# Kernel optimization log

Hardware: AMD Instinct MI355X
Metric: run time of the kernel (lower is better)

The kernel has to match this reference:

```python
import jax, jax.numpy as jnp
import numpy as np


def setup_inputs() -> dict:
    key = jax.random.key(0)
    ks = jax.random.split(key, 5)
    B, S, D, H, E = 2, 2048, 1024, 2816, 8
    x = jax.random.normal(ks[0], (B, S, D), dtype=jnp.float32)
    Wg = jax.random.normal(ks[1], (E, D), dtype=jnp.float32) * 0.02
    W1 = jax.random.normal(ks[2], (E, H, D), dtype=jnp.float32) * 0.02
    W2 = jax.random.normal(ks[3], (E, H, D), dtype=jnp.float32) * 0.02
    W3 = jax.random.normal(ks[4], (E, D, H), dtype=jnp.float32) * 0.02
    return {"x": x, "Wg": Wg, "W1": W1, "W2": W2, "W3": W3}


TOP_K = 2


def reference(x, Wg, W1, W2, W3):
    B, S, D = x.shape
    E = Wg.shape[0]
    xt = x.reshape(B * S, D)  # [T, D]
    # gating: raw logits, NO softmax (matches original module)
    scores = xt @ Wg.T  # [T, E]
    topk_scores, topk_idx = jax.lax.top_k(scores, TOP_K)  # [T, K]
    # dense per-expert SwiGLU FFN over all tokens, combined with sparse weights
    gate = jax.nn.silu(jnp.einsum('td,ehd->teh', xt, W1))  # [T, E, H]
    up = jnp.einsum('td,ehd->teh', xt, W2)                 # [T, E, H]
    y = jnp.einsum('teh,edh->ted', gate * up, W3)           # [T, E, D]
    # combine weights: w[t, e] = sum_k topk_scores[t, k] * (topk_idx[t, k] == e)
    onehot = jax.nn.one_hot(topk_idx, E, dtype=x.dtype)     # [T, K, E]
    w = jnp.einsum('tke,tk->te', onehot, topk_scores)       # [T, E]
    out = jnp.einsum('te,ted->td', w, y)                    # [T, D]
    return out.reshape(B, S, D)
```

## Files before the change

kernel.cpp:

```cpp
#include <hip/hip_runtime.h>
#include <hip/hip_bf16.h>
#include <stdint.h>


#define T_TOK 4096
#define DDIM 1024
#define HDIM 2816
#define NEXP 8

typedef __attribute__((ext_vector_type(8))) short short8;
typedef __attribute__((ext_vector_type(4))) short short4v;
typedef __attribute__((ext_vector_type(4))) float floatx4;

__device__ __forceinline__ short f2bf(float f) {
  union { float f; unsigned int u; } v; v.f = f;
  unsigned int u = v.u;
  u += 0x7FFFu + ((u >> 16) & 1u);
  return (short)(u >> 16);
}

__device__ __forceinline__ void gl2lds16(const void* g, void* l) {
  __builtin_amdgcn_global_load_lds(
      (const __attribute__((address_space(1))) void*)g,
      (__attribute__((address_space(3))) void*)l, 16, 0, 0);
}

#define CONV_ELEM4 5767168
__global__ __launch_bounds__(256) void convert_kernel(
    const float* __restrict__ W1, const float* __restrict__ W2, const float* __restrict__ W3,
    short* __restrict__ W1bf, short* __restrict__ W2bf, short* __restrict__ W3bf) {
  int z = blockIdx.y;
  const float4* src = (const float4*)((z == 0) ? W1 : (z == 1) ? W2 : W3);
  short4v* dst = (short4v*)((z == 0) ? W1bf : (z == 1) ? W2bf : W3bf);
  size_t stride = (size_t)gridDim.x * 256;
  for (size_t i = (size_t)blockIdx.x * 256 + threadIdx.x; i < CONV_ELEM4; i += stride) {
    float4 v = src[i];
    dst[i] = (short4v){f2bf(v.x), f2bf(v.y), f2bf(v.z), f2bf(v.w)};
  }
}

__global__ __launch_bounds__(256) void gating_score_kernel(const float* __restrict__ x,
    const float* __restrict__ Wg, short* __restrict__ xbf,
    int* __restrict__ re, float* __restrict__ rw) {
  int t = blockIdx.x * 4 + (threadIdx.x >> 6);
  int lane = threadIdx.x & 63;
  const float* xt = x + (size_t)t * DDIM;
  float xr[16];
#pragma unroll
  for (int j = 0; j < 16; ++j) xr[j] = xt[j * 64 + lane];
  short* xbt = xbf + (size_t)t * DDIM;
#pragma unroll
  for (int j = 0; j < 16; ++j) xbt[j * 64 + lane] = f2bf(xr[j]);
  float s[NEXP];
#pragma unroll
  for (int e = 0; e < NEXP; ++e) {
    const float* wge = Wg + e * DDIM;
    float p = 0.f;
#pragma unroll
    for (int j = 0; j < 16; ++j) p += xr[j] * wge[j * 64 + lane];
#pragma unroll
    for (int o = 32; o > 0; o >>= 1) p += __shfl_xor(p, o, 64);
    s[e] = p;
  }
  if (lane == 0) {
    int e1 = 0; float s1 = s[0];
#pragma unroll
    for (int e = 1; e < NEXP; ++e) if (s[e] > s1) { s1 = s[e]; e1 = e; }
    int e2 = -1; float s2 = -1e30f;
#pragma unroll
    for (int e = 0; e < NEXP; ++e) if (e != e1 && s[e] > s2) { s2 = s[e]; e2 = e; }
    re[2 * t] = e1;     rw[2 * t] = s1;
    re[2 * t + 1] = e2; rw[2 * t + 1] = s2;
  }
}

__global__ __launch_bounds__(1024) void route_kernel(const int* __restrict__ re,
    int* __restrict__ counts, int* __restrict__ offs,
    int* __restrict__ rs, int* __restrict__ tlist) {
  __shared__ int H[NEXP * 1024];
  __shared__ int totS[NEXP];
  int tid = threadIdx.x;
  int myre[8];
  int cnt[NEXP];
#pragma unroll
  for (int e = 0; e < NEXP; ++e) cnt[e] = 0;
  const int4* re4 = (const int4*)(re + tid * 8);
  int4 a = re4[0], b = re4[1];
  myre[0] = a.x; myre[1] = a.y; myre[2] = a.z; myre[3] = a.w;
  myre[4] = b.x; myre[5] = b.y; myre[6] = b.z; myre[7] = b.w;
#pragma unroll
  for (int j = 0; j < 8; ++j) cnt[myre[j]]++;
#pragma unroll
  for (int e = 0; e < NEXP; ++e) H[e * 1024 + tid] = cnt[e];
  __syncthreads();
  int wave = tid >> 6, lane = tid & 63;
  if (wave < NEXP) {
    int run = 0;
    for (int c = 0; c < 16; ++c) {
      int i = c * 64 + lane;
      int v = H[wave * 1024 + i];
      int sc = v;
#pragma unroll
      for (int o = 1; o < 64; o <<= 1) {
        int u = __shfl_up(sc, o, 64);
        if (lane >= o) sc += u;
      }
      int tot = __shfl(sc, 63, 64);
      H[wave * 1024 + i] = run + sc - v;
      run += tot;
    }
    if (lane == 0) totS[wave] = run;
  }
  __syncthreads();
  if (tid == 0) {
    int run = 0;
    for (int e = 0; e < NEXP; ++e) {
      offs[e] = run; counts[e] = totS[e]; run += totS[e];
    }
  }
  int pos[NEXP];
#pragma unroll
  for (int e = 0; e < NEXP; ++e) pos[e] = H[e * 1024 + tid];
#pragma unroll
  for (int j = 0; j < 8; ++j) {
    int e = myre[j];
    int slot = pos[e]++;
    int idx = tid * 8 + j;
    rs[idx] = slot;
    tlist[e * T_TOK + slot] = idx >> 1;
  }
}

__global__ __launch_bounds__(256) void ffn1_fast_kernel(const short* __restrict__ xbf,
    const short* __restrict__ W1bf, const short* __restrict__ W2bf,
    const int* __restrict__ counts, const int* __restrict__ offs,
    const int* __restrict__ tlist, short* __restrict__ hmat) {
  int e = blockIdx.z;
  int cnt = counts[e];
  int m0 = blockIdx.y * 128;
  if (m0 >= cnt) return;
  int n0 = blockIdx.x * 64;
  __shared__ __attribute__((aligned(16))) short As[128 * 64];
  __shared__ __attribute__((aligned(16))) short Bs1[64 * 64];
  __shared__ __attribute__((aligned(16))) short Bs2[64 * 64];
  __shared__ int toks[128];
  int tid = threadIdx.x;
  if (tid < 128) {
    int m = m0 + tid;
    toks[tid] = tlist[e * T_TOK + (m < cnt ? m : cnt - 1)];
  }
  __syncthreads();
  int lane = tid & 63, w = tid >> 6;
  int wr = w >> 1, wc = w & 1;
  int lrow = lane & 15, lq = lane >> 4;
  int sr = lane >> 3;
  int sc = lane & 7;
  int scs = ((sc ^ sr) & 7) * 8;
  const short* pA[4];
#pragma unroll
  for (int j = 0; j < 4; ++j)
    pA[j] = xbf + (size_t)toks[w * 32 + j * 8 + sr] * DDIM + scs;
  const short* b1e = W1bf + (size_t)e * HDIM * DDIM;
  const short* b2e = W2bf + (size_t)e * HDIM * DDIM;
  const short* pB1[2]; const short* pB2[2];
#pragma unroll
  for (int j = 0; j < 2; ++j) {
    int row = w * 16 + j * 8 + sr;
    pB1[j] = b1e + (size_t)(n0 + row) * DDIM + scs;
    pB2[j] = b2e + (size_t)(n0 + row) * DDIM + scs;
  }
  void* lA[4]; void* lB1[2]; void* lB2[2];
#pragma unroll
  for (int j = 0; j < 4; ++j) lA[j] = (void*)&As[(w * 32 + j * 8) * 64];
#pragma unroll
  for (int j = 0; j < 2; ++j) {
    lB1[j] = (void*)&Bs1[(w * 16 + j * 8) * 64];
    lB2[j] = (void*)&Bs2[(w * 16 + j * 8) * 64];
  }
  floatx4 accg[4][2], accu[4][2];
#pragma unroll
  for (int i = 0; i < 4; ++i)
#pragma unroll
    for (int j = 0; j < 2; ++j) {
      accg[i][j] = (floatx4){0.f, 0.f, 0.f, 0.f};
      accu[i][j] = (floatx4){0.f, 0.f, 0.f, 0.f};
    }
  for (int kk = 0; kk < DDIM; kk += 64) {
#pragma unroll
    for (int j = 0; j < 4; ++j) { gl2lds16(pA[j], lA[j]); pA[j] += 64; }
#pragma unroll
    for (int j = 0; j < 2; ++j) {
      gl2lds16(pB1[j], lB1[j]); pB1[j] += 64;
      gl2lds16(pB2[j], lB2[j]); pB2[j] += 64;
    }
    __syncthreads();
#pragma unroll
    for (int kh = 0; kh < 2; ++kh) {
      int csw = (((kh * 4 + lq) ^ (lrow & 7)) & 7) * 8;
      short8 a[4], b1[2], b2[2];
#pragma unroll
      for (int mf = 0; mf < 4; ++mf)
        a[mf] = *(short8*)&As[(wr * 64 + mf * 16 + lrow) * 64 + csw];
#pragma unroll
      for (int nf = 0; nf < 2; ++nf) {
        b1[nf] = *(short8*)&Bs1[(wc * 32 + nf * 16 + lrow) * 64 + csw];
        b2[nf] = *(short8*)&Bs2[(wc * 32 + nf * 16 + lrow) * 64 + csw];
      }
#pragma unroll
      for (int mf = 0; mf < 4; ++mf)
#pragma unroll
        for (int nf = 0; nf < 2; ++nf) {
          accg[mf][nf] = __builtin_amdgcn_mfma_f32_16x16x32_bf16(a[mf], b1[nf], accg[mf][nf], 0, 0, 0);
          accu[mf][nf] = __builtin_amdgcn_mfma_f32_16x16x32_bf16(a[mf], b2[nf], accu[mf][nf], 0, 0, 0);
        }
    }
    __syncthreads();
  }
  int base = offs[e];
#pragma unroll
  for (int mf = 0; mf < 4; ++mf)
#pragma unroll
    for (int r = 0; r < 4; ++r) {
      int mloc = wr * 64 + mf * 16 + lq * 4 + r;
      if (m0 + mloc < cnt) {
        size_t row = (size_t)(base + m0 + mloc);
#pragma unroll
        for (int nf = 0; nf < 2; ++nf) {
          float g = accg[mf][nf][r];
          float u = accu[mf][nf][r];
          float h = g / (1.f + __expf(-g)) * u;
          hmat[row * HDIM + n0 + wc * 32 + nf * 16 + lrow] = f2bf(h);
        }
      }
    }
}

#define KSPLIT 2
#define KHALF (HDIM / KSPLIT)
__global__ __launch_bounds__(256) void ffn2_fast_kernel(const short* __restrict__ hmat,
    const short* __restrict__ W3bf,
    const int* __restrict__ counts, const int* __restrict__ offs,
    float* __restrict__ ypart0, float* __restrict__ ypart1) {
  int e = blockIdx.z;
  int cnt = counts[e];
  int m0 = blockIdx.y * 128;
  if (m0 >= cnt) return;
  int ks = blockIdx.x >> 3;
  int n0 = (blockIdx.x & 7) * 128;
  int k0 = ks * KHALF;
  float* ypart = ks ? ypart1 : ypart0;
  int base = offs[e];
  __shared__ __attribute__((aligned(16))) short As[128 * 64];
  __shared__ __attribute__((aligned(16))) short Bs[128 * 64];
  int tid = threadIdx.x;
  int lane = tid & 63, w = tid >> 6;
  int wr = w >> 1, wc = w & 1;
  int lrow = lane & 15, lq = lane >> 4;
  int sr = lane >> 3;
  int sc = lane & 7;
  int scs = ((sc ^ sr) & 7) * 8;
  const short* W3e = W3bf + (size_t)e * DDIM * HDIM;
  const short* pA[4]; const short* pB[4];
  void* lA[4]; void* lB[4];
#pragma unroll
  for (int j = 0; j < 4; ++j) {
    int gr = m0 + w * 32 + j * 8 + sr;
    gr = gr < cnt ? gr : cnt - 1;
    pA[j] = hmat + (size_t)(base + gr) * HDIM + k0 + scs;
    pB[j] = W3e + (size_t)(n0 + w * 32 + j * 8 + sr) * HDIM + k0 + scs;
    lA[j] = (void*)&As[(w * 32 + j * 8) * 64];
    lB[j] = (void*)&Bs[(w * 32 + j * 8) * 64];
  }
  floatx4 acc[4][4];
#pragma unroll
  for (int i = 0; i < 4; ++i)
#pragma unroll
    for (int j = 0; j < 4; ++j) acc[i][j] = (floatx4){0.f, 0.f, 0.f, 0.f};
  for (int kk = 0; kk < KHALF; kk += 64) {
#pragma unroll
    for (int j = 0; j < 4; ++j) { gl2lds16(pA[j], lA[j]); pA[j] += 64; }
#pragma unroll
    for (int j = 0; j < 4; ++j) { gl2lds16(pB[j], lB[j]); pB[j] += 64; }
    __syncthreads();
#pragma unroll
    for (int kh = 0; kh < 2; ++kh) {
      int csw = (((kh * 4 + lq) ^ (lrow & 7)) & 7) * 8;
      short8 a[4], b[4];
#pragma unroll
      for (int mf = 0; mf < 4; ++mf)
        a[mf] = *(short8*)&As[(wr * 64 + mf * 16 + lrow) * 64 + csw];
#pragma unroll
      for (int nf = 0; nf < 4; ++nf)
        b[nf] = *(short8*)&Bs[(wc * 64 + nf * 16 + lrow) * 64 + csw];
#pragma unroll
      for (int mf = 0; mf < 4; ++mf)
#pragma unroll
        for (int nf = 0; nf < 4; ++nf)
          acc[mf][nf] = __builtin_amdgcn_mfma_f32_16x16x32_bf16(a[mf], b[nf], acc[mf][nf], 0, 0, 0);
    }
    __syncthreads();
  }
#pragma unroll
  for (int mf = 0; mf < 4; ++mf)
#pragma unroll
    for (int r = 0; r < 4; ++r) {
      int mloc = wr * 64 + mf * 16 + lq * 4 + r;
      if (m0 + mloc < cnt) {
        float* orow = ypart + (size_t)(base + m0 + mloc) * DDIM + n0 + wc * 64 + lrow;
#pragma unroll
        for (int nf = 0; nf < 4; ++nf)
          orow[nf * 16] = acc[mf][nf][r];
      }
    }
}

__global__ __launch_bounds__(256) void combine_kernel(const float4* __restrict__ y0,
    const float4* __restrict__ y1,
    const int* __restrict__ offs, const int* __restrict__ re, const int* __restrict__ rs,
    const float* __restrict__ rw, float4* __restrict__ out4) {
  int t = blockIdx.x;
  int i = threadIdx.x;
  size_t r0 = (size_t)(offs[re[2 * t]] + rs[2 * t]) * 256 + i;
  size_t r1 = (size_t)(offs[re[2 * t + 1]] + rs[2 * t + 1]) * 256 + i;
  float w0 = rw[2 * t], w1 = rw[2 * t + 1];
  float4 a0 = y0[r0], a1 = y1[r0];
  float4 b0 = y0[r1], b1 = y1[r1];
  out4[(size_t)t * 256 + i] = make_float4(
      w0 * (a0.x + a1.x) + w1 * (b0.x + b1.x),
      w0 * (a0.y + a1.y) + w1 * (b0.y + b1.y),
      w0 * (a0.z + a1.z) + w1 * (b0.z + b1.z),
      w0 * (a0.w + a1.w) + w1 * (b0.w + b1.w));
}

extern "C" void kernel_launch(void* const* d_in, const int* in_sizes, int n_in,
                              void* d_out, int out_size, void* d_ws, size_t ws_size,
                              hipStream_t stream) {
  const float* x  = (const float*)d_in[0];
  const float* Wg = (const float*)d_in[1];
  const float* W1 = (const float*)d_in[2];
  const float* W2 = (const float*)d_in[3];
  const float* W3 = (const float*)d_in[4];
  float* out = (float*)d_out;
  char* ws = (char*)d_ws;

  int*   counts = (int*)(ws + 0);
  int*   offs   = (int*)(ws + 256);
  int*   tlist  = (int*)(ws + 512);
  int*   re     = (int*)(ws + 131584);
  int*   rs     = (int*)(ws + 164352);
  float* rw     = (float*)(ws + 197120);
  short* xbf    = (short*)(ws + 229888);
  short* hmat   = (short*)(ws + 8618496);
  short* W3bf   = (short*)(ws + 54755840);
  short* W1bf   = (short*)(ws + 100893184);
  short* W2bf   = (short*)(ws + 147030528);
  float* ypart0 = (float*)(ws + 100893184);
  float* ypart1 = (float*)(ws + 147030528);

  convert_kernel<<<dim3(4096, 3), 256, 0, stream>>>(W1, W2, W3, W1bf, W2bf, W3bf);
  gating_score_kernel<<<T_TOK / 4, 256, 0, stream>>>(x, Wg, xbf, re, rw);
  route_kernel<<<1, 1024, 0, stream>>>(re, counts, offs, rs, tlist);
  ffn1_fast_kernel<<<dim3(HDIM / 64, T_TOK / 128, NEXP), 256, 0, stream>>>(
      xbf, W1bf, W2bf, counts, offs, tlist, hmat);
  ffn2_fast_kernel<<<dim3((DDIM / 128) * KSPLIT, T_TOK / 128, NEXP), 256, 0, stream>>>(
      hmat, W3bf, counts, offs, ypart0, ypart1);
  combine_kernel<<<T_TOK, 256, 0, stream>>>((const float4*)ypart0, (const float4*)ypart1,
                                            offs, re, rs, rw, (float4*)out);
}
```

Before: 528.6 us.

## Triple-buffer LDS pipeline with 512-thread blocks and larger tiles in FFN GEMMs

Both grouped-expert GEMM kernels move to 512-thread blocks with wider N tiles (128 for ffn1, 256 for ffn2). They use a three-stage LDS ring buffer in which global-to-LDS loads for tile t+2 are issued while tile t is computed. Explicit vmcnt waits and split barriers replace the per-iteration __syncthreads pairs, and setprio is raised around the MFMA bursts. The goal is to hide global load latency and improve operand reuse per block. The cost is larger LDS use per block (about 144KB), which may limit occupancy, and more fragile hand-written synchronisation.

Measured after the change: 623.4 us. 17.9% more time.

```diff
diff --git a/kernel.cpp b/kernel.cpp
--- a/kernel.cpp
+++ b/kernel.cpp
@@ -131,7 +131,8 @@
   }
 }
 
-__global__ __launch_bounds__(256) void ffn1_fast_kernel(const short* __restrict__ xbf,
+#define F1_NT 16
+__global__ __launch_bounds__(512) void ffn1_fast_kernel(const short* __restrict__ xbf,
     const short* __restrict__ W1bf, const short* __restrict__ W2bf,
     const int* __restrict__ counts, const int* __restrict__ offs,
     const int* __restrict__ tlist, short* __restrict__ hmat) {
@@ -139,10 +140,8 @@
   int cnt = counts[e];
   int m0 = blockIdx.y * 128;
   if (m0 >= cnt) return;
-  int n0 = blockIdx.x * 64;
-  __shared__ __attribute__((aligned(16))) short As[128 * 64];
-  __shared__ __attribute__((aligned(16))) short Bs1[64 * 64];
-  __shared__ __attribute__((aligned(16))) short Bs2[64 * 64];
+  int n0 = blockIdx.x * 128;
+  __shared__ __attribute__((aligned(16))) short lds[3 * 24576];
   __shared__ int toks[128];
   int tid = threadIdx.x;
   if (tid < 128) {
@@ -151,31 +150,20 @@
   }
   __syncthreads();
   int lane = tid & 63, w = tid >> 6;
-  int wr = w >> 1, wc = w & 1;
+  int wr = w >> 2, wc = w & 3;
   int lrow = lane & 15, lq = lane >> 4;
   int sr = lane >> 3;
-  int sc = lane & 7;
-  int scs = ((sc ^ sr) & 7) * 8;
-  const short* pA[4];
-#pragma unroll
-  for (int j = 0; j < 4; ++j)
-    pA[j] = xbf + (size_t)toks[w * 32 + j * 8 + sr] * DDIM + scs;
+  int scs = (((lane & 7) ^ sr) & 7) * 8;
+  int w8 = w * 8;
   const short* b1e = W1bf + (size_t)e * HDIM * DDIM;
   const short* b2e = W2bf + (size_t)e * HDIM * DDIM;
-  const short* pB1[2]; const short* pB2[2];
-#pragma unroll
-  for (int j = 0; j < 2; ++j) {
-    int row = w * 16 + j * 8 + sr;
-    pB1[j] = b1e + (size_t)(n0 + row) * DDIM + scs;
-    pB2[j] = b2e + (size_t)(n0 + row) * DDIM + scs;
-  }
-  void* lA[4]; void* lB1[2]; void* lB2[2];
-#pragma unroll
-  for (int j = 0; j < 4; ++j) lA[j] = (void*)&As[(w * 32 + j * 8) * 64];
-#pragma unroll
-  for (int j = 0; j < 2; ++j) {
-    lB1[j] = (void*)&Bs1[(w * 16 + j * 8) * 64];
-    lB2[j] = (void*)&Bs2[(w * 16 + j * 8) * 64];
+  const short* pA[2]; const short* pB1[2]; const short* pB2[2];
+#pragma unroll
+  for (int r = 0; r < 2; ++r) {
+    pA[r] = xbf + (size_t)toks[r * 64 + w8 + sr] * DDIM + scs;
+    int grow = n0 + r * 64 + w8 + sr;
+    pB1[r] = b1e + (size_t)grow * DDIM + scs;
+    pB2[r] = b2e + (size_t)grow * DDIM + scs;
   }
   floatx4 accg[4][2], accu[4][2];
 #pragma unroll
@@ -185,36 +173,78 @@
       accg[i][j] = (floatx4){0.f, 0.f, 0.f, 0.f};
       accu[i][j] = (floatx4){0.f, 0.f, 0.f, 0.f};
     }
-  for (int kk = 0; kk < DDIM; kk += 64) {
-#pragma unroll
-    for (int j = 0; j < 4; ++j) { gl2lds16(pA[j], lA[j]); pA[j] += 64; }
-#pragma unroll
-    for (int j = 0; j < 2; ++j) {
-      gl2lds16(pB1[j], lB1[j]); pB1[j] += 64;
-      gl2lds16(pB2[j], lB2[j]); pB2[j] += 64;
-    }
-    __syncthreads();
-#pragma unroll
-    for (int kh = 0; kh < 2; ++kh) {
-      int csw = (((kh * 4 + lq) ^ (lrow & 7)) & 7) * 8;
-      short8 a[4], b1[2], b2[2];
-#pragma unroll
-      for (int mf = 0; mf < 4; ++mf)
-        a[mf] = *(short8*)&As[(wr * 64 + mf * 16 + lrow) * 64 + csw];
+  {
+    short* bufp = lds;
+#pragma unroll
+    for (int b = 0; b < 2; ++b) {
+#pragma unroll
+      for (int p = 0; p < 2; ++p) {
+        gl2lds16(pA[p],  (void*)(bufp + (p * 64 + w8) * 64));
+        gl2lds16(pB1[p], (void*)(bufp + 8192 + (p * 64 + w8) * 64));
+        gl2lds16(pB2[p], (void*)(bufp + 16384 + (p * 64 + w8) * 64));
+        pA[p] += 64; pB1[p] += 64; pB2[p] += 64;
+      }
+      bufp += 24576;
+    }
+  }
+  asm volatile("s_waitcnt vmcnt(6)" ::: "memory");
+  __builtin_amdgcn_s_barrier();
+  int rsel = 0, wsel = 2;
+  for (int t = 0; t < F1_NT; ++t) {
+    const short* Ab = lds + rsel * 24576;
+    const short* B1b = Ab + 8192;
+    const short* B2b = Ab + 16384;
+    short* Wb = lds + wsel * 24576;
+#pragma unroll
+    for (int mh = 0; mh < 2; ++mh) {
+      if (t < F1_NT - 2) {
+        gl2lds16(pA[mh],  (void*)(Wb + (mh * 64 + w8) * 64));
+        gl2lds16(pB1[mh], (void*)(Wb + 8192 + (mh * 64 + w8) * 64));
+        gl2lds16(pB2[mh], (void*)(Wb + 16384 + (mh * 64 + w8) * 64));
+        pA[mh] += 64; pB1[mh] += 64; pB2[mh] += 64;
+      }
+      short8 a[2][2], b1v[2][2], b2v[2][2];
+#pragma unroll
+      for (int mf2 = 0; mf2 < 2; ++mf2) {
+        int arow = wr * 64 + mh * 32 + mf2 * 16 + lrow;
+#pragma unroll
+        for (int kh = 0; kh < 2; ++kh) {
+          int csw = (((kh * 4 + lq) ^ (lrow & 7)) & 7) * 8;
+          a[mf2][kh] = *(const short8*)&Ab[arow * 64 + csw];
+        }
+      }
 #pragma unroll
       for (int nf = 0; nf < 2; ++nf) {
-        b1[nf] = *(short8*)&Bs1[(wc * 32 + nf * 16 + lrow) * 64 + csw];
-        b2[nf] = *(short8*)&Bs2[(wc * 32 + nf * 16 + lrow) * 64 + csw];
-      }
-#pragma unroll
-      for (int mf = 0; mf < 4; ++mf)
-#pragma unroll
-        for (int nf = 0; nf < 2; ++nf) {
-          accg[mf][nf] = __builtin_amdgcn_mfma_f32_16x16x32_bf16(a[mf], b1[nf], accg[mf][nf], 0, 0, 0);
-          accu[mf][nf] = __builtin_amdgcn_mfma_f32_16x16x32_bf16(a[mf], b2[nf], accu[mf][nf], 0, 0, 0);
+        int brow = wc * 32 + nf * 16 + lrow;
+#pragma unroll
+        for (int kh = 0; kh < 2; ++kh) {
+          int csw = (((kh * 4 + lq) ^ (lrow & 7)) & 7) * 8;
+          b1v[nf][kh] = *(const short8*)&B1b[brow * 64 + csw];
+          b2v[nf][kh] = *(const short8*)&B2b[brow * 64 + csw];
         }
-    }
-    __syncthreads();
+      }
+      __builtin_amdgcn_s_barrier();
+      __builtin_amdgcn_s_setprio(1);
+#pragma unroll
+      for (int mf2 = 0; mf2 < 2; ++mf2)
+#pragma unroll
+        for (int nf = 0; nf < 2; ++nf)
+#pragma unroll
+          for (int kh = 0; kh < 2; ++kh) {
+            accg[mh * 2 + mf2][nf] = __builtin_amdgcn_mfma_f32_16x16x32_bf16(
+                a[mf2][kh], b1v[nf][kh], accg[mh * 2 + mf2][nf], 0, 0, 0);
+            accu[mh * 2 + mf2][nf] = __builtin_amdgcn_mfma_f32_16x16x32_bf16(
+                a[mf2][kh], b2v[nf][kh], accu[mh * 2 + mf2][nf], 0, 0, 0);
+          }
+      __builtin_amdgcn_s_setprio(0);
+      if (mh == 1) {
+        if (t < F1_NT - 2)      asm volatile("s_waitcnt vmcnt(6)" ::: "memory");
+        else if (t == F1_NT - 2) asm volatile("s_waitcnt vmcnt(0)" ::: "memory");
+      }
+      __builtin_amdgcn_s_barrier();
+    }
+    rsel = (rsel == 2) ? 0 : rsel + 1;
+    wsel = (wsel == 2) ? 0 : wsel + 1;
   }
   int base = offs[e];
 #pragma unroll
@@ -237,7 +267,8 @@
 
 #define KSPLIT 2
 #define KHALF (HDIM / KSPLIT)
-__global__ __launch_bounds__(256) void ffn2_fast_kernel(const short* __restrict__ hmat,
+#define F2_NT 22
+__global__ __launch_bounds__(512) void ffn2_fast_kernel(const short* __restrict__ hmat,
     const short* __restrict__ W3bf,
     const int* __restrict__ counts, const int* __restrict__ offs,
     float* __restrict__ ypart0, float* __restrict__ ypart1) {
@@ -245,60 +276,99 @@
   int cnt = counts[e];
   int m0 = blockIdx.y * 128;
   if (m0 >= cnt) return;
-  int ks = blockIdx.x >> 3;
-  int n0 = (blockIdx.x & 7) * 128;
+  int ks = blockIdx.x >> 2;
+  int n0 = (blockIdx.x & 3) * 256;
   int k0 = ks * KHALF;
   float* ypart = ks ? ypart1 : ypart0;
   int base = offs[e];
-  __shared__ __attribute__((aligned(16))) short As[128 * 64];
-  __shared__ __attribute__((aligned(16))) short Bs[128 * 64];
+  __shared__ __attribute__((aligned(16))) short lds[3 * 24576];
   int tid = threadIdx.x;
   int lane = tid & 63, w = tid >> 6;
-  int wr = w >> 1, wc = w & 1;
+  int wr = w >> 2, wc = w & 3;
   int lrow = lane & 15, lq = lane >> 4;
   int sr = lane >> 3;
-  int sc = lane & 7;
-  int scs = ((sc ^ sr) & 7) * 8;
+  int scs = (((lane & 7) ^ sr) & 7) * 8;
+  int w8 = w * 8;
   const short* W3e = W3bf + (size_t)e * DDIM * HDIM;
-  const short* pA[4]; const short* pB[4];
-  void* lA[4]; void* lB[4];
-#pragma unroll
-  for (int j = 0; j < 4; ++j) {
-    int gr = m0 + w * 32 + j * 8 + sr;
+  const short* pA[2]; const short* pB[4];
+#pragma unroll
+  for (int r = 0; r < 2; ++r) {
+    int gr = m0 + r * 64 + w8 + sr;
     gr = gr < cnt ? gr : cnt - 1;
-    pA[j] = hmat + (size_t)(base + gr) * HDIM + k0 + scs;
-    pB[j] = W3e + (size_t)(n0 + w * 32 + j * 8 + sr) * HDIM + k0 + scs;
-    lA[j] = (void*)&As[(w * 32 + j * 8) * 64];
-    lB[j] = (void*)&Bs[(w * 32 + j * 8) * 64];
-  }
+    pA[r] = hmat + (size_t)(base + gr) * HDIM + k0 + scs;
+  }
+#pragma unroll
+  for (int r = 0; r < 4; ++r)
+    pB[r] = W3e + (size_t)(n0 + r * 64 + w8 + sr) * HDIM + k0 + scs;
   floatx4 acc[4][4];
 #pragma unroll
   for (int i = 0; i < 4; ++i)
 #pragma unroll
     for (int j = 0; j < 4; ++j) acc[i][j] = (floatx4){0.f, 0.f, 0.f, 0.f};
-  for (int kk = 0; kk < KHALF; kk += 64) {
-#pragma unroll
-    for (int j = 0; j < 4; ++j) { gl2lds16(pA[j], lA[j]); pA[j] += 64; }
-#pragma unroll
-    for (int j = 0; j < 4; ++j) { gl2lds16(pB[j], lB[j]); pB[j] += 64; }
-    __syncthreads();
-#pragma unroll
-    for (int kh = 0; kh < 2; ++kh) {
-      int csw = (((kh * 4 + lq) ^ (lrow & 7)) & 7) * 8;
-      short8 a[4], b[4];
-#pragma unroll
-      for (int mf = 0; mf < 4; ++mf)
-        a[mf] = *(short8*)&As[(wr * 64 + mf * 16 + lrow) * 64 + csw];
-#pragma unroll
-      for (int nf = 0; nf < 4; ++nf)
-        b[nf] = *(short8*)&Bs[(wc * 64 + nf * 16 + lrow) * 64 + csw];
-#pragma unroll
-      for (int mf = 0; mf < 4; ++mf)
+  {
+    short* bufp = lds;
+#pragma unroll
+    for (int b = 0; b < 2; ++b) {
+#pragma unroll
+      for (int r = 0; r < 2; ++r) { gl2lds16(pA[r], (void*)(bufp + (r * 64 + w8) * 64)); pA[r] += 64; }
+#pragma unroll
+      for (int r = 0; r < 4; ++r) { gl2lds16(pB[r], (void*)(bufp + 8192 + (r * 64 + w8) * 64)); pB[r] += 64; }
+      bufp += 24576;
+    }
+  }
+  asm volatile("s_waitcnt vmcnt(6)" ::: "memory");
+  __builtin_amdgcn_s_barrier();
+  int rsel = 0, wsel = 2;
+  for (int t = 0; t < F2_NT; ++t) {
+    const short* Ab = lds + rsel * 24576;
+    const short* Bb = Ab + 8192;
+    short* Wb = lds + wsel * 24576;
+#pragma unroll
+    for (int mh = 0; mh < 2; ++mh) {
+      if (t < F2_NT - 2) {
+        gl2lds16(pA[mh], (void*)(Wb + (mh * 64 + w8) * 64));
+        gl2lds16(pB[2 * mh],     (void*)(Wb + 8192 + ((2 * mh) * 64 + w8) * 64));
+        gl2lds16(pB[2 * mh + 1], (void*)(Wb + 8192 + ((2 * mh + 1) * 64 + w8) * 64));
+        pA[mh] += 64; pB[2 * mh] += 64; pB[2 * mh + 1] += 64;
+      }
+      short8 a[2][2], bv[4][2];
+#pragma unroll
+      for (int mf2 = 0; mf2 < 2; ++mf2) {
+        int arow = wr * 64 + mh * 32 + mf2 * 16 + lrow;
+#pragma unroll
+        for (int kh = 0; kh < 2; ++kh) {
+          int csw = (((kh * 4 + lq) ^ (lrow & 7)) & 7) * 8;
+          a[mf2][kh] = *(const short8*)&Ab[arow * 64 + csw];
+        }
+      }
+#pragma unroll
+      for (int nf = 0; nf < 4; ++nf) {
+        int brow = wc * 64 + nf * 16 + lrow;
+#pragma unroll
+        for (int kh = 0; kh < 2; ++kh) {
+          int csw = (((kh * 4 + lq) ^ (lrow & 7)) & 7) * 8;
+          bv[nf][kh] = *(const short8*)&Bb[brow * 64 + csw];
+        }
+      }
+      __builtin_amdgcn_s_barrier();
+      __builtin_amdgcn_s_setprio(1);
+#pragma unroll
+      for (int mf2 = 0; mf2 < 2; ++mf2)
 #pragma unroll
         for (int nf = 0; nf < 4; ++nf)
-          acc[mf][nf] = __builtin_amdgcn_mfma_f32_16x16x32_bf16(a[mf], b[nf], acc[mf][nf], 0, 0, 0);
-    }
-    __syncthreads();
+#pragma unroll
+          for (int kh = 0; kh < 2; ++kh)
+            acc[mh * 2 + mf2][nf] = __builtin_amdgcn_mfma_f32_16x16x32_bf16(
+                a[mf2][kh], bv[nf][kh], acc[mh * 2 + mf2][nf], 0, 0, 0);
+      __builtin_amdgcn_s_setprio(0);
+      if (mh == 1) {
+        if (t < F2_NT - 2)       asm volatile("s_waitcnt vmcnt(6)" ::: "memory");
+        else if (t == F2_NT - 2) asm volatile("s_waitcnt vmcnt(0)" ::: "memory");
+      }
+      __builtin_amdgcn_s_barrier();
+    }
+    rsel = (rsel == 2) ? 0 : rsel + 1;
+    wsel = (wsel == 2) ? 0 : wsel + 1;
   }
 #pragma unroll
   for (int mf = 0; mf < 4; ++mf)
@@ -360,9 +430,9 @@
   convert_kernel<<<dim3(4096, 3), 256, 0, stream>>>(W1, W2, W3, W1bf, W2bf, W3bf);
   gating_score_kernel<<<T_TOK / 4, 256, 0, stream>>>(x, Wg, xbf, re, rw);
   route_kernel<<<1, 1024, 0, stream>>>(re, counts, offs, rs, tlist);
-  ffn1_fast_kernel<<<dim3(HDIM / 64, T_TOK / 128, NEXP), 256, 0, stream>>>(
+  ffn1_fast_kernel<<<dim3(HDIM / 128, T_TOK / 128, NEXP), 512, 0, stream>>>(
       xbf, W1bf, W2bf, counts, offs, tlist, hmat);
-  ffn2_fast_kernel<<<dim3((DDIM / 128) * KSPLIT, T_TOK / 128, NEXP), 256, 0, stream>>>(
+  ffn2_fast_kernel<<<dim3((DDIM / 256) * KSPLIT, T_TOK / 128, NEXP), 512, 0, stream>>>(
       hmat, W3bf, counts, offs, ypart0, ypart1);
   combine_kernel<<<T_TOK, 256, 0, stream>>>((const float4*)ypart0, (const float4*)ypart1,
                                             offs, re, rs, rw, (float4*)out);
```

## Double-buffer LDS in both FFN GEMMs and fuse combine into ffn2 via atomics

Applied to the files above, without the earlier changes.

Both expert GEMM kernels now use two LDS buffers, so the global-to-LDS loads for the next K tile are issued while the current tile is being multiplied, which aims to hide memory latency. The ffn2 kernel no longer writes per-split partial outputs. It scales its accumulators by the routing weight and atomically adds them straight into the zeroed output, which removes the combine kernel and the partial-buffer round trip. The cost is float atomic traffic, a memset, doubled LDS use that may lower occupancy, and a summation order that is no longer deterministic.

New measurement: 573.5 us. 1.09x slower.

```diff
diff --git a/kernel.cpp b/kernel.cpp
--- a/kernel.cpp
+++ b/kernel.cpp
@@ -131,6 +131,7 @@
   }
 }
 
+#define F1_NT 16
 __global__ __launch_bounds__(256) void ffn1_fast_kernel(const short* __restrict__ xbf,
     const short* __restrict__ W1bf, const short* __restrict__ W2bf,
     const int* __restrict__ counts, const int* __restrict__ offs,
@@ -140,9 +141,9 @@
   int m0 = blockIdx.y * 128;
   if (m0 >= cnt) return;
   int n0 = blockIdx.x * 64;
-  __shared__ __attribute__((aligned(16))) short As[128 * 64];
-  __shared__ __attribute__((aligned(16))) short Bs1[64 * 64];
-  __shared__ __attribute__((aligned(16))) short Bs2[64 * 64];
+  __shared__ __attribute__((aligned(16))) short As[2][128 * 64];
+  __shared__ __attribute__((aligned(16))) short Bs1[2][64 * 64];
+  __shared__ __attribute__((aligned(16))) short Bs2[2][64 * 64];
   __shared__ int toks[128];
   int tid = threadIdx.x;
   if (tid < 128) {
@@ -154,8 +155,7 @@
   int wr = w >> 1, wc = w & 1;
   int lrow = lane & 15, lq = lane >> 4;
   int sr = lane >> 3;
-  int sc = lane & 7;
-  int scs = ((sc ^ sr) & 7) * 8;
+  int scs = (((lane & 7) ^ sr) & 7) * 8;
   const short* pA[4];
 #pragma unroll
   for (int j = 0; j < 4; ++j)
@@ -169,14 +169,6 @@
     pB1[j] = b1e + (size_t)(n0 + row) * DDIM + scs;
     pB2[j] = b2e + (size_t)(n0 + row) * DDIM + scs;
   }
-  void* lA[4]; void* lB1[2]; void* lB2[2];
-#pragma unroll
-  for (int j = 0; j < 4; ++j) lA[j] = (void*)&As[(w * 32 + j * 8) * 64];
-#pragma unroll
-  for (int j = 0; j < 2; ++j) {
-    lB1[j] = (void*)&Bs1[(w * 16 + j * 8) * 64];
-    lB2[j] = (void*)&Bs2[(w * 16 + j * 8) * 64];
-  }
   floatx4 accg[4][2], accu[4][2];
 #pragma unroll
   for (int i = 0; i < 4; ++i)
@@ -185,26 +177,34 @@
       accg[i][j] = (floatx4){0.f, 0.f, 0.f, 0.f};
       accu[i][j] = (floatx4){0.f, 0.f, 0.f, 0.f};
     }
-  for (int kk = 0; kk < DDIM; kk += 64) {
-#pragma unroll
-    for (int j = 0; j < 4; ++j) { gl2lds16(pA[j], lA[j]); pA[j] += 64; }
-#pragma unroll
-    for (int j = 0; j < 2; ++j) {
-      gl2lds16(pB1[j], lB1[j]); pB1[j] += 64;
-      gl2lds16(pB2[j], lB2[j]); pB2[j] += 64;
-    }
-    __syncthreads();
+#define F1_STAGE(buf)                                                        \
+  do {                                                                       \
+    _Pragma("unroll")                                                        \
+    for (int j = 0; j < 4; ++j) {                                            \
+      gl2lds16(pA[j], (void*)&As[buf][(w * 32 + j * 8) * 64]); pA[j] += 64;  \
+    }                                                                        \
+    _Pragma("unroll")                                                        \
+    for (int j = 0; j < 2; ++j) {                                            \
+      gl2lds16(pB1[j], (void*)&Bs1[buf][(w * 16 + j * 8) * 64]); pB1[j] += 64; \
+      gl2lds16(pB2[j], (void*)&Bs2[buf][(w * 16 + j * 8) * 64]); pB2[j] += 64; \
+    }                                                                        \
+  } while (0)
+  F1_STAGE(0);
+  __syncthreads();
+  for (int t = 0; t < F1_NT; ++t) {
+    int cur = t & 1;
+    if (t < F1_NT - 1) F1_STAGE(cur ^ 1);
 #pragma unroll
     for (int kh = 0; kh < 2; ++kh) {
       int csw = (((kh * 4 + lq) ^ (lrow & 7)) & 7) * 8;
       short8 a[4], b1[2], b2[2];
 #pragma unroll
       for (int mf = 0; mf < 4; ++mf)
-        a[mf] = *(short8*)&As[(wr * 64 + mf * 16 + lrow) * 64 + csw];
+        a[mf] = *(const short8*)&As[cur][(wr * 64 + mf * 16 + lrow) * 64 + csw];
 #pragma unroll
       for (int nf = 0; nf < 2; ++nf) {
-        b1[nf] = *(short8*)&Bs1[(wc * 32 + nf * 16 + lrow) * 64 + csw];
-        b2[nf] = *(short8*)&Bs2[(wc * 32 + nf * 16 + lrow) * 64 + csw];
+        b1[nf] = *(const short8*)&Bs1[cur][(wc * 32 + nf * 16 + lrow) * 64 + csw];
+        b2[nf] = *(const short8*)&Bs2[cur][(wc * 32 + nf * 16 + lrow) * 64 + csw];
       }
 #pragma unroll
       for (int mf = 0; mf < 4; ++mf)
@@ -237,10 +237,12 @@
 
 #define KSPLIT 2
 #define KHALF (HDIM / KSPLIT)
+#define F2_NT 22
 __global__ __launch_bounds__(256) void ffn2_fast_kernel(const short* __restrict__ hmat,
     const short* __restrict__ W3bf,
     const int* __restrict__ counts, const int* __restrict__ offs,
-    float* __restrict__ ypart0, float* __restrict__ ypart1) {
+    const int* __restrict__ tlist, const int* __restrict__ re,
+    const float* __restrict__ rw, float* __restrict__ out) {
   int e = blockIdx.z;
   int cnt = counts[e];
   int m0 = blockIdx.y * 128;
@@ -248,50 +250,61 @@
   int ks = blockIdx.x >> 3;
   int n0 = (blockIdx.x & 7) * 128;
   int k0 = ks * KHALF;
-  float* ypart = ks ? ypart1 : ypart0;
   int base = offs[e];
-  __shared__ __attribute__((aligned(16))) short As[128 * 64];
-  __shared__ __attribute__((aligned(16))) short Bs[128 * 64];
+  __shared__ __attribute__((aligned(16))) short As[2][128 * 64];
+  __shared__ __attribute__((aligned(16))) short Bs[2][128 * 64];
+  __shared__ int toksS[128];
+  __shared__ float wS[128];
   int tid = threadIdx.x;
+  if (tid < 128) {
+    int m = m0 + tid;
+    int t = tlist[e * T_TOK + (m < cnt ? m : cnt - 1)];
+    toksS[tid] = t;
+    wS[tid] = (re[2 * t] == e) ? rw[2 * t] : rw[2 * t + 1];
+  }
+  __syncthreads();
   int lane = tid & 63, w = tid >> 6;
   int wr = w >> 1, wc = w & 1;
   int lrow = lane & 15, lq = lane >> 4;
   int sr = lane >> 3;
-  int sc = lane & 7;
-  int scs = ((sc ^ sr) & 7) * 8;
+  int scs = (((lane & 7) ^ sr) & 7) * 8;
   const short* W3e = W3bf + (size_t)e * DDIM * HDIM;
   const short* pA[4]; const short* pB[4];
-  void* lA[4]; void* lB[4];
 #pragma unroll
   for (int j = 0; j < 4; ++j) {
     int gr = m0 + w * 32 + j * 8 + sr;
     gr = gr < cnt ? gr : cnt - 1;
     pA[j] = hmat + (size_t)(base + gr) * HDIM + k0 + scs;
     pB[j] = W3e + (size_t)(n0 + w * 32 + j * 8 + sr) * HDIM + k0 + scs;
-    lA[j] = (void*)&As[(w * 32 + j * 8) * 64];
-    lB[j] = (void*)&Bs[(w * 32 + j * 8) * 64];
   }
   floatx4 acc[4][4];
 #pragma unroll
   for (int i = 0; i < 4; ++i)
 #pragma unroll
     for (int j = 0; j < 4; ++j) acc[i][j] = (floatx4){0.f, 0.f, 0.f, 0.f};
-  for (int kk = 0; kk < KHALF; kk += 64) {
-#pragma unroll
-    for (int j = 0; j < 4; ++j) { gl2lds16(pA[j], lA[j]); pA[j] += 64; }
-#pragma unroll
-    for (int j = 0; j < 4; ++j) { gl2lds16(pB[j], lB[j]); pB[j] += 64; }
-    __syncthreads();
+#define F2_STAGE(buf)                                                        \
+  do {                                                                       \
+    _Pragma("unroll")                                                        \
+    for (int j = 0; j < 4; ++j) {                                            \
+      gl2lds16(pA[j], (void*)&As[buf][(w * 32 + j * 8) * 64]); pA[j] += 64;  \
+      gl2lds16(pB[j], (void*)&Bs[buf][(w * 32 + j * 8) * 64]); pB[j] += 64;  \
+    }                                                                        \
+  } while (0)
+  F2_STAGE(0);
+  __syncthreads();
+  for (int t = 0; t < F2_NT; ++t) {
+    int cur = t & 1;
+    if (t < F2_NT - 1) F2_STAGE(cur ^ 1);
 #pragma unroll
     for (int kh = 0; kh < 2; ++kh) {
       int csw = (((kh * 4 + lq) ^ (lrow & 7)) & 7) * 8;
       short8 a[4], b[4];
 #pragma unroll
       for (int mf = 0; mf < 4; ++mf)
-        a[mf] = *(short8*)&As[(wr * 64 + mf * 16 + lrow) * 64 + csw];
+        a[mf] = *(const short8*)&As[cur][(wr * 64 + mf * 16 + lrow) * 64 + csw];
 #pragma unroll
       for (int nf = 0; nf < 4; ++nf)
-        b[nf] = *(short8*)&Bs[(wc * 64 + nf * 16 + lrow) * 64 + csw];
+        b[nf] = *(const short8*)&Bs[cur][(wc * 64 + nf * 16 + lrow) * 64 + csw];
 #pragma unroll
       for (int mf = 0; mf < 4; ++mf)
 #pragma unroll
@@ -306,30 +319,14 @@
     for (int r = 0; r < 4; ++r) {
       int mloc = wr * 64 + mf * 16 + lq * 4 + r;
       if (m0 + mloc < cnt) {
-        float* orow = ypart + (size_t)(base + m0 + mloc) * DDIM + n0 + wc * 64 + lrow;
+        int tok = toksS[mloc];
+        float wgt = wS[mloc];
+        float* orow = out + (size_t)tok * DDIM + n0 + wc * 64 + lrow;
 #pragma unroll
         for (int nf = 0; nf < 4; ++nf)
-          orow[nf * 16] = acc[mf][nf][r];
+          unsafeAtomicAdd(orow + nf * 16, wgt * acc[mf][nf][r]);
       }
     }
-}
-
-__global__ __launch_bounds__(256) void combine_kernel(const float4* __restrict__ y0,
-    const float4* __restrict__ y1,
-    const int* __restrict__ offs, const int* __restrict__ re, const int* __restrict__ rs,
-    const float* __restrict__ rw, float4* __restrict__ out4) {
-  int t = blockIdx.x;
-  int i = threadIdx.x;
-  size_t r0 = (size_t)(offs[re[2 * t]] + rs[2 * t]) * 256 + i;
-  size_t r1 = (size_t)(offs[re[2 * t + 1]] + rs[2 * t + 1]) * 256 + i;
-  float w0 = rw[2 * t], w1 = rw[2 * t + 1];
-  float4 a0 = y0[r0], a1 = y1[r0];
-  float4 b0 = y0[r1], b1 = y1[r1];
-  out4[(size_t)t * 256 + i] = make_float4(
-      w0 * (a0.x + a1.x) + w1 * (b0.x + b1.x),
-      w0 * (a0.y + a1.y) + w1 * (b0.y + b1.y),
-      w0 * (a0.z + a1.z) + w1 * (b0.z + b1.z),
-      w0 * (a0.w + a1.w) + w1 * (b0.w + b1.w));
 }
 
 extern "C" void kernel_launch(void* const* d_in, const int* in_sizes, int n_in,
@@ -354,16 +351,13 @@
   short* W3bf   = (short*)(ws + 54755840);
   short* W1bf   = (short*)(ws + 100893184);
   short* W2bf   = (short*)(ws + 147030528);
-  float* ypart0 = (float*)(ws + 100893184);
-  float* ypart1 = (float*)(ws + 147030528);
-
+
+  hipMemsetAsync(out, 0, out_size, stream);
   convert_kernel<<<dim3(4096, 3), 256, 0, stream>>>(W1, W2, W3, W1bf, W2bf, W3bf);
   gating_score_kernel<<<T_TOK / 4, 256, 0, stream>>>(x, Wg, xbf, re, rw);
   route_kernel<<<1, 1024, 0, stream>>>(re, counts, offs, rs, tlist);
   ffn1_fast_kernel<<<dim3(HDIM / 64, T_TOK / 128, NEXP), 256, 0, stream>>>(
       xbf, W1bf, W2bf, counts, offs, tlist, hmat);
   ffn2_fast_kernel<<<dim3((DDIM / 128) * KSPLIT, T_TOK / 128, NEXP), 256, 0, stream>>>(
-      hmat, W3bf, counts, offs, ypart0, ypart1);
-  combine_kernel<<<T_TOK, 256, 0, stream>>>((const float4*)ypart0, (const float4*)ypart1,
-                                            offs, re, rs, rw, (float4*)out);
-}
+      hmat, W3bf, counts, offs, tlist, re, rw, out);
+}
```
